# Kernel optimization log

Hardware: AMD Instinct MI355X
Metric: run time of the kernel (lower is better)

Reference implementation:

```python
import jax, jax.numpy as jnp
import numpy as np

B, L, D, V = 64, 512, 768, 100
LN_EPS = 1e-6


def setup_inputs() -> dict:
    key = jax.random.key(0)
    k1, k2, k3, k4 = jax.random.split(key, 4)
    return {
        "ids": jax.random.randint(k1, (B, 1), 0, V),
        "pooler": jax.random.normal(k2, (B, L, D), dtype=jnp.float32),
        "emb_table": jax.random.normal(k3, (V, 2), dtype=jnp.float32),
        "W_dense": jax.random.normal(k4, (2, D), dtype=jnp.float32) * 0.1,
        "b_dense": jnp.zeros((D,), dtype=jnp.float32),
        "gamma": jnp.ones((D,), dtype=jnp.float32),
        "beta": jnp.zeros((D,), dtype=jnp.float32),
    }


def reference(ids, pooler, emb_table, W_dense, b_dense, gamma, beta):
    # id -> 2-dim projection -> dense to embed_dim: xt (B, 1, D)
    emb = emb_table[ids]                      # (B, 1, 2)
    xt = emb @ W_dense + b_dense              # (B, 1, D)

    # Per timestep i the original concatenates [pooler[:, i], xt] into a
    # 2-token sequence and runs dot-product self-attention (keras Attention,
    # no scaling), then sums over the 2 tokens. Vectorized over all L steps:
    tok = jnp.stack([pooler, jnp.broadcast_to(xt, pooler.shape)], axis=2)  # (B, L, 2, D)
    scores = jnp.einsum('blqd,blkd->blqk', tok, tok)                       # (B, L, 2, 2)
    attn = jax.nn.softmax(scores, axis=-1)
    out = jnp.einsum('blqk,blkd->blqd', attn, tok)                         # (B, L, 2, D)
    summed = out.sum(axis=2)                                               # (B, L, D)

    # dropout is identity at inference; layernorm over last axis, eps=1e-6
    mean = summed.mean(axis=-1, keepdims=True)
    var = summed.var(axis=-1, keepdims=True)
    normed = (summed - mean) * jax.lax.rsqrt(var + LN_EPS)
    return normed * gamma + beta
```

## Files before the change

kernel.cpp:

```cpp
#include <hip/hip_runtime.h>


constexpr int Bc = 64;
constexpr int Lc = 512;
constexpr int Dc = 768;
constexpr float LN_EPS = 1e-6f;
constexpr int WAVES_PER_BLOCK = 4;
constexpr int ROWS_PER_WAVE   = 4;
constexpr int ROWS_PER_BLOCK  = WAVES_PER_BLOCK * ROWS_PER_WAVE;

typedef float nv_float4 __attribute__((ext_vector_type(4)));

__global__ __launch_bounds__(64 * WAVES_PER_BLOCK) void hier_attn_ln_kernel(
    const int*   __restrict__ ids,
    const float* __restrict__ pooler,
    const float* __restrict__ emb_table,
    const float* __restrict__ W,
    const float* __restrict__ bvec,
    const float* __restrict__ gamma,
    const float* __restrict__ beta,
    float*       __restrict__ out)
{
    const int wave = threadIdx.x >> 6;
    const int lane = threadIdx.x & 63;
    const int row0 = blockIdx.x * ROWS_PER_BLOCK + wave * ROWS_PER_WAVE;
    const int b    = row0 >> 9;

    const float4* W0_4 = (const float4*)W;
    const float4* W1_4 = (const float4*)(W + Dc);
    const float4* b_4  = (const float4*)bvec;
    const float4* g_4  = (const float4*)gamma;
    const float4* be_4 = (const float4*)beta;

    const int id = ids[b];
    const float e0 = emb_table[id * 2 + 0];
    const float e1 = emb_table[id * 2 + 1];

    float4 xt[3], gm[3], bt[3];
    float s11 = 0.f, S1 = 0.f;
#pragma unroll
    for (int j = 0; j < 3; ++j) {
        const int idx4 = lane + j * 64;
        float4 w0 = W0_4[idx4];
        float4 w1 = W1_4[idx4];
        float4 bd = b_4[idx4];
        gm[j] = g_4[idx4];
        bt[j] = be_4[idx4];
        float4 x;
        x.x = fmaf(e0, w0.x, fmaf(e1, w1.x, bd.x));
        x.y = fmaf(e0, w0.y, fmaf(e1, w1.y, bd.y));
        x.z = fmaf(e0, w0.z, fmaf(e1, w1.z, bd.z));
        x.w = fmaf(e0, w0.w, fmaf(e1, w1.w, bd.w));
        xt[j] = x;
        s11 += x.x*x.x + x.y*x.y + x.z*x.z + x.w*x.w;
        S1  += x.x + x.y + x.z + x.w;
    }
#pragma unroll
    for (int off = 32; off > 0; off >>= 1) {
        s11 += __shfl_xor(s11, off);
        S1  += __shfl_xor(S1,  off);
    }

    const float invD = 1.f / (float)Dc;
    const float4* p_base = (const float4*)(pooler + (size_t)row0 * Dc);
    nv_float4*    o_base = (nv_float4*)(out + (size_t)row0 * Dc);

#pragma unroll
    for (int r = 0; r < ROWS_PER_WAVE; ++r) {
        const float4* prow4 = p_base + (size_t)r * (Dc / 4);
        nv_float4*    orow4 = o_base + (size_t)r * (Dc / 4);

        float4 t0[3];
        float s00 = 0.f, s01 = 0.f, S0 = 0.f;
#pragma unroll
        for (int j = 0; j < 3; ++j) {
            float4 p = prow4[lane + j * 64];
            t0[j] = p;
            s00 += p.x*p.x + p.y*p.y + p.z*p.z + p.w*p.w;
            s01 += p.x*xt[j].x + p.y*xt[j].y + p.z*xt[j].z + p.w*xt[j].w;
            S0  += p.x + p.y + p.z + p.w;
        }
#pragma unroll
        for (int off = 32; off > 0; off >>= 1) {
            s00 += __shfl_xor(s00, off);
            s01 += __shfl_xor(s01, off);
            S0  += __shfl_xor(S0,  off);
        }

        const float m0  = fmaxf(s00, s01);
        const float a00 = __expf(s00 - m0);
        const float a01 = __expf(s01 - m0);
        const float r0  = 1.f / (a00 + a01);
        const float m1  = fmaxf(s01, s11);
        const float a10 = __expf(s01 - m1);
        const float a11 = __expf(s11 - m1);
        const float r1  = 1.f / (a10 + a11);
        const float w0s = a00 * r0 + a10 * r1;
        const float w1s = a01 * r0 + a11 * r1;

        const float mean = (w0s * S0 + w1s * S1) * invD;
        const float ex2  = (w0s*w0s*s00 + 2.f*w0s*w1s*s01 + w1s*w1s*s11) * invD;
        const float var  = ex2 - mean * mean;
        const float rstd = rsqrtf(var + LN_EPS);

        const float a = w0s * rstd;
        const float c = w1s * rstd;
        const float m = mean * rstd;

#pragma unroll
        for (int j = 0; j < 3; ++j) {
            nv_float4 o;
            o.x = fmaf(gm[j].x, fmaf(a, t0[j].x, fmaf(c, xt[j].x, -m)), bt[j].x);
            o.y = fmaf(gm[j].y, fmaf(a, t0[j].y, fmaf(c, xt[j].y, -m)), bt[j].y);
            o.z = fmaf(gm[j].z, fmaf(a, t0[j].z, fmaf(c, xt[j].z, -m)), bt[j].z);
            o.w = fmaf(gm[j].w, fmaf(a, t0[j].w, fmaf(c, xt[j].w, -m)), bt[j].w);
            __builtin_nontemporal_store(o, &orow4[lane + j * 64]);
        }
    }
}

extern "C" void kernel_launch(void* const* d_in, const int* in_sizes, int n_in,
                              void* d_out, int out_size, void* d_ws, size_t ws_size,
                              hipStream_t stream) {
    const int*   ids       = (const int*)  d_in[0];
    const float* pooler    = (const float*)d_in[1];
    const float* emb_table = (const float*)d_in[2];
    const float* W_dense   = (const float*)d_in[3];
    const float* b_dense   = (const float*)d_in[4];
    const float* gamma     = (const float*)d_in[5];
    const float* beta      = (const float*)d_in[6];
    float* out = (float*)d_out;

    const int nrows = Bc * Lc;
    hipLaunchKernelGGL(hier_attn_ln_kernel,
                       dim3(nrows / ROWS_PER_BLOCK), dim3(64 * WAVES_PER_BLOCK),
                       0, stream,
                       ids, pooler, emb_table, W_dense, b_dense, gamma, beta, out);
}
```

Before: 193.9 us.

## Software-prefetch next rows via double-buffered registers and LDS staging, 8 rows per wave

Restructures the per-wave row loop to issue loads for the next pair of pooler rows before finishing the current rows, staging consumed rows in shared memory. Rows per wave increase from 4 to 8, halving the grid, and launch bounds request 4 blocks per CU. The aim is to hide global load latency in this bandwidth-bound layernorm kernel. It adds LDS traffic and reduces the number of blocks, which may lower memory-level parallelism.

After: 194.9 us. Within noise of the previous version (+0.5%).

```diff
diff --git a/kernel.cpp b/kernel.cpp
--- a/kernel.cpp
+++ b/kernel.cpp
@@ -4,14 +4,15 @@
 constexpr int Bc = 64;
 constexpr int Lc = 512;
 constexpr int Dc = 768;
+constexpr int NF4 = Dc / 4;
 constexpr float LN_EPS = 1e-6f;
-constexpr int WAVES_PER_BLOCK = 4;
-constexpr int ROWS_PER_WAVE   = 4;
-constexpr int ROWS_PER_BLOCK  = WAVES_PER_BLOCK * ROWS_PER_WAVE;
+constexpr int WPB = 4;
+constexpr int RPW = 8;
+constexpr int RPB = WPB * RPW;
 
 typedef float nv_float4 __attribute__((ext_vector_type(4)));
 
-__global__ __launch_bounds__(64 * WAVES_PER_BLOCK) void hier_attn_ln_kernel(
+__global__ __launch_bounds__(64 * WPB, 4) void hier_attn_ln_kernel(
     const int*   __restrict__ ids,
     const float* __restrict__ pooler,
     const float* __restrict__ emb_table,
@@ -21,9 +22,12 @@
     const float* __restrict__ beta,
     float*       __restrict__ out)
 {
+    __shared__ float4 tile[WPB][2][NF4];
+
     const int wave = threadIdx.x >> 6;
     const int lane = threadIdx.x & 63;
-    const int row0 = blockIdx.x * ROWS_PER_BLOCK + wave * ROWS_PER_WAVE;
+    const int wid  = blockIdx.x * WPB + wave;
+    const int row0 = wid * RPW;
     const int b    = row0 >> 9;
 
     const float4* W0_4 = (const float4*)W;
@@ -40,12 +44,10 @@
     float s11 = 0.f, S1 = 0.f;
 #pragma unroll
     for (int j = 0; j < 3; ++j) {
-        const int idx4 = lane + j * 64;
-        float4 w0 = W0_4[idx4];
-        float4 w1 = W1_4[idx4];
-        float4 bd = b_4[idx4];
-        gm[j] = g_4[idx4];
-        bt[j] = be_4[idx4];
+        const int i4 = lane + j * 64;
+        float4 w0 = W0_4[i4], w1 = W1_4[i4], bd = b_4[i4];
+        gm[j] = g_4[i4];
+        bt[j] = be_4[i4];
         float4 x;
         x.x = fmaf(e0, w0.x, fmaf(e1, w1.x, bd.x));
         x.y = fmaf(e0, w0.y, fmaf(e1, w1.y, bd.y));
@@ -65,58 +67,84 @@
     const float4* p_base = (const float4*)(pooler + (size_t)row0 * Dc);
     nv_float4*    o_base = (nv_float4*)(out + (size_t)row0 * Dc);
 
-#pragma unroll
-    for (int r = 0; r < ROWS_PER_WAVE; ++r) {
-        const float4* prow4 = p_base + (size_t)r * (Dc / 4);
-        nv_float4*    orow4 = o_base + (size_t)r * (Dc / 4);
+#define CONSUME(Q0, Q1, Q2, SLOT, A0, A1, A2)                                   \
+    do {                                                                        \
+        A0  = Q0.x*Q0.x + Q0.y*Q0.y + Q0.z*Q0.z + Q0.w*Q0.w;                    \
+        A1  = Q0.x*xt[0].x + Q0.y*xt[0].y + Q0.z*xt[0].z + Q0.w*xt[0].w;        \
+        A2  = Q0.x + Q0.y + Q0.z + Q0.w;                                        \
+        A0 += Q1.x*Q1.x + Q1.y*Q1.y + Q1.z*Q1.z + Q1.w*Q1.w;                    \
+        A1 += Q1.x*xt[1].x + Q1.y*xt[1].y + Q1.z*xt[1].z + Q1.w*xt[1].w;        \
+        A2 += Q1.x + Q1.y + Q1.z + Q1.w;                                        \
+        A0 += Q2.x*Q2.x + Q2.y*Q2.y + Q2.z*Q2.z + Q2.w*Q2.w;                    \
+        A1 += Q2.x*xt[2].x + Q2.y*xt[2].y + Q2.z*xt[2].z + Q2.w*xt[2].w;        \
+        A2 += Q2.x + Q2.y + Q2.z + Q2.w;                                        \
+        tile[wave][SLOT][lane]       = Q0;                                      \
+        tile[wave][SLOT][lane + 64]  = Q1;                                      \
+        tile[wave][SLOT][lane + 128] = Q2;                                      \
+    } while (0)
 
-        float4 t0[3];
-        float s00 = 0.f, s01 = 0.f, S0 = 0.f;
-#pragma unroll
-        for (int j = 0; j < 3; ++j) {
-            float4 p = prow4[lane + j * 64];
-            t0[j] = p;
-            s00 += p.x*p.x + p.y*p.y + p.z*p.z + p.w*p.w;
-            s01 += p.x*xt[j].x + p.y*xt[j].y + p.z*xt[j].z + p.w*xt[j].w;
-            S0  += p.x + p.y + p.z + p.w;
+#define FINISH(SLOT, R, A0, A1, A2)                                             \
+    do {                                                                        \
+        _Pragma("unroll")                                                       \
+        for (int off = 32; off > 0; off >>= 1) {                                \
+            A0 += __shfl_xor(A0, off);                                          \
+            A1 += __shfl_xor(A1, off);                                          \
+            A2 += __shfl_xor(A2, off);                                          \
+        }                                                                       \
+        const float m0  = fmaxf(A0, A1);                                        \
+        const float x00 = __expf(A0 - m0);                                      \
+        const float x01 = __expf(A1 - m0);                                      \
+        const float r0_ = 1.f / (x00 + x01);                                    \
+        const float m1  = fmaxf(A1, s11);                                       \
+        const float x10 = __expf(A1 - m1);                                      \
+        const float x11 = __expf(s11 - m1);                                     \
+        const float r1_ = 1.f / (x10 + x11);                                    \
+        const float w0s = x00 * r0_ + x10 * r1_;                                \
+        const float w1s = x01 * r0_ + x11 * r1_;                                \
+        const float mean = (w0s * A2 + w1s * S1) * invD;                        \
+        const float ex2  = (w0s*w0s*A0 + 2.f*w0s*w1s*A1 + w1s*w1s*s11) * invD;  \
+        const float rstd = rsqrtf(ex2 - mean * mean + LN_EPS);                  \
+        const float pa = w0s * rstd, pc = w1s * rstd, pm = mean * rstd;         \
+        nv_float4* orow = o_base + (size_t)(R) * NF4;                           \
+        _Pragma("unroll")                                                       \
+        for (int j = 0; j < 3; ++j) {                                           \
+            const float4 p = tile[wave][SLOT][lane + j * 64];                   \
+            nv_float4 o;                                                        \
+            o.x = fmaf(gm[j].x, fmaf(pa, p.x, fmaf(pc, xt[j].x, -pm)), bt[j].x);\
+            o.y = fmaf(gm[j].y, fmaf(pa, p.y, fmaf(pc, xt[j].y, -pm)), bt[j].y);\
+            o.z = fmaf(gm[j].z, fmaf(pa, p.z, fmaf(pc, xt[j].z, -pm)), bt[j].z);\
+            o.w = fmaf(gm[j].w, fmaf(pa, p.w, fmaf(pc, xt[j].w, -pm)), bt[j].w);\
+            __builtin_nontemporal_store(o, &orow[lane + j * 64]);               \
+        }                                                                       \
+    } while (0)
+
+    float4 qa0 = p_base[lane],        qa1 = p_base[lane + 64],
+           qa2 = p_base[lane + 128];
+    float4 qb0 = p_base[NF4 + lane],  qb1 = p_base[NF4 + lane + 64],
+           qb2 = p_base[NF4 + lane + 128];
+
+#pragma unroll 1
+    for (int it = 0; it < RPW / 2; ++it) {
+        const int r0 = 2 * it;
+        const bool more = (it < RPW / 2 - 1);
+        float a0, a1, a2;
+
+        CONSUME(qa0, qa1, qa2, 0, a0, a1, a2);
+        if (more) {
+            const float4* nb = p_base + (size_t)(r0 + 2) * NF4;
+            qa0 = nb[lane]; qa1 = nb[lane + 64]; qa2 = nb[lane + 128];
         }
-#pragma unroll
-        for (int off = 32; off > 0; off >>= 1) {
-            s00 += __shfl_xor(s00, off);
-            s01 += __shfl_xor(s01, off);
-            S0  += __shfl_xor(S0,  off);
+        FINISH(0, r0, a0, a1, a2);
+
+        CONSUME(qb0, qb1, qb2, 1, a0, a1, a2);
+        if (more) {
+            const float4* nb = p_base + (size_t)(r0 + 3) * NF4;
+            qb0 = nb[lane]; qb1 = nb[lane + 64]; qb2 = nb[lane + 128];
         }
-
-        const float m0  = fmaxf(s00, s01);
-        const float a00 = __expf(s00 - m0);
-        const float a01 = __expf(s01 - m0);
-        const float r0  = 1.f / (a00 + a01);
-        const float m1  = fmaxf(s01, s11);
-        const float a10 = __expf(s01 - m1);
-        const float a11 = __expf(s11 - m1);
-        const float r1  = 1.f / (a10 + a11);
-        const float w0s = a00 * r0 + a10 * r1;
-        const float w1s = a01 * r0 + a11 * r1;
-
-        const float mean = (w0s * S0 + w1s * S1) * invD;
-        const float ex2  = (w0s*w0s*s00 + 2.f*w0s*w1s*s01 + w1s*w1s*s11) * invD;
-        const float var  = ex2 - mean * mean;
-        const float rstd = rsqrtf(var + LN_EPS);
-
-        const float a = w0s * rstd;
-        const float c = w1s * rstd;
-        const float m = mean * rstd;
-
-#pragma unroll
-        for (int j = 0; j < 3; ++j) {
-            nv_float4 o;
-            o.x = fmaf(gm[j].x, fmaf(a, t0[j].x, fmaf(c, xt[j].x, -m)), bt[j].x);
-            o.y = fmaf(gm[j].y, fmaf(a, t0[j].y, fmaf(c, xt[j].y, -m)), bt[j].y);
-            o.z = fmaf(gm[j].z, fmaf(a, t0[j].z, fmaf(c, xt[j].z, -m)), bt[j].z);
-            o.w = fmaf(gm[j].w, fmaf(a, t0[j].w, fmaf(c, xt[j].w, -m)), bt[j].w);
-            __builtin_nontemporal_store(o, &orow4[lane + j * 64]);
-        }
+        FINISH(1, r0 + 1, a0, a1, a2);
     }
+#undef CONSUME
+#undef FINISH
 }
 
 extern "C" void kernel_launch(void* const* d_in, const int* in_sizes, int n_in,
@@ -133,7 +161,7 @@
 
     const int nrows = Bc * Lc;
     hipLaunchKernelGGL(hier_attn_ln_kernel,
-                       dim3(nrows / ROWS_PER_BLOCK), dim3(64 * WAVES_PER_BLOCK),
+                       dim3(nrows / RPB), dim3(64 * WPB),
                        0, stream,
                        ids, pooler, emb_table, W_dense, b_dense, gamma, beta, out);
 }
```
